# Performance work log

Measured on AMD Instinct MI355X. Metric: run time of the kernel, lower is better.

Reference implementation:

```python
import jax, jax.numpy as jnp
import numpy as np


def setup_inputs() -> dict:
    key = jax.random.key(0)
    k1, k2, k3 = jax.random.split(key, 3)
    B, N, M = 64, 1024, 1024
    src = jax.random.normal(k1, (B, 3, N), dtype=jnp.float32)
    tgt = jax.random.normal(k2, (B, 3, M), dtype=jnp.float32)
    scores = jax.random.normal(k3, (B, N, M), dtype=jnp.float32)
    return {"src": src, "tgt": tgt, "scores": scores}


def reference(src, tgt, scores):
    # softmax over the tgt-point axis (dim=2 in torch)
    p = jax.nn.softmax(scores, axis=2)                       # [B,N,M]
    # src_corr = tgt @ scores^T  -> soft correspondences in tgt for each src point
    src_corr = jnp.einsum('bdm,bnm->bdn', tgt, p)            # [B,3,N]
    src_mean = src.mean(axis=2, keepdims=True)               # [B,3,1]
    corr_mean = src_corr.mean(axis=2, keepdims=True)         # [B,3,1]
    src_c = src - src_mean
    corr_c = src_corr - corr_mean
    # cross-covariance H = src_centered @ src_corr_centered^T  -> [B,3,3]
    H = jnp.einsum('bdn,ben->bde', src_c, corr_c)
    U, S, Vh = jnp.linalg.svd(H)                             # batched 3x3 SVD
    V = jnp.swapaxes(Vh, -1, -2)
    Ut = jnp.swapaxes(U, -1, -2)
    R0 = V @ Ut                                              # candidate rotation
    det = jnp.linalg.det(R0)                                 # [B]
    # reflection fix: flip last column of V where det < 0 (reflect = diag(1,1,-1))
    flip = jnp.where(det < 0, -1.0, 1.0)                     # [B]
    ones = jnp.ones_like(flip)
    col_scale = jnp.stack([ones, ones, flip], axis=-1)[:, None, :]  # [B,1,3]
    R = (V * col_scale) @ Ut                                 # [B,3,3]
    t = (-R @ src_mean) + corr_mean                          # [B,3,1]
    return R, t.reshape(src.shape[0], 3)
```

## Files before the change

### kernel.cpp

```cpp
#include <hip/hip_runtime.h>
#include <math.h>

#define BATCH 64
#define NPTS  1024
#define MPTS  1024
#define ROWS_PER_BLOCK 8
#define BLOCKS_PER_BATCH (NPTS / ROWS_PER_BLOCK)

__global__ __launch_bounds__(512) void softmax_stats_kernel(
    const float* __restrict__ src,
    const float* __restrict__ tgt,
    const float* __restrict__ scores,
    float* __restrict__ partials)
{
    __shared__ float tgt_lds[3 * MPTS];
    __shared__ float part[ROWS_PER_BLOCK][16];

    const int tid  = threadIdx.x;
    const int lane = tid & 63;
    const int wave = tid >> 6;
    const int row0 = blockIdx.x * ROWS_PER_BLOCK;
    const int b    = row0 >> 10;

    {
        const float4* tgt4 = (const float4*)(tgt + (size_t)b * 3 * MPTS);
        float4* lds4 = (float4*)tgt_lds;
        for (int idx = tid; idx < 768; idx += 512)
            lds4[idx] = tgt4[idx];
    }
    __syncthreads();

    const int r = row0 + wave;
    const int n = r & (NPTS - 1);
    const float4* srow = (const float4*)(scores + (size_t)r * MPTS);

    float sum = 0.f, w0 = 0.f, w1 = 0.f, w2 = 0.f;
    float4 v[4];
    #pragma unroll
    for (int k = 0; k < 4; ++k) v[k] = srow[k * 64 + lane];
    #pragma unroll
    for (int k = 0; k < 4; ++k) {
        const int m4 = k * 64 + lane;
        float e0 = __expf(v[k].x);
        float e1 = __expf(v[k].y);
        float e2 = __expf(v[k].z);
        float e3 = __expf(v[k].w);
        sum += e0 + e1 + e2 + e3;
        float4 t0 = ((const float4*)(tgt_lds + 0 * MPTS))[m4];
        float4 t1 = ((const float4*)(tgt_lds + 1 * MPTS))[m4];
        float4 t2 = ((const float4*)(tgt_lds + 2 * MPTS))[m4];
        w0 += e0 * t0.x + e1 * t0.y + e2 * t0.z + e3 * t0.w;
        w1 += e0 * t1.x + e1 * t1.y + e2 * t1.z + e3 * t1.w;
        w2 += e0 * t2.x + e1 * t2.y + e2 * t2.z + e3 * t2.w;
    }
    #pragma unroll
    for (int off = 32; off >= 1; off >>= 1) {
        sum += __shfl_xor(sum, off);
        w0  += __shfl_xor(w0, off);
        w1  += __shfl_xor(w1, off);
        w2  += __shfl_xor(w2, off);
    }

    if (lane == 0) {
        const float inv = 1.0f / sum;
        const float c0 = w0 * inv, c1 = w1 * inv, c2 = w2 * inv;
        const float s0 = src[((size_t)b * 3 + 0) * NPTS + n];
        const float s1 = src[((size_t)b * 3 + 1) * NPTS + n];
        const float s2 = src[((size_t)b * 3 + 2) * NPTS + n];
        float* p = part[wave];
        p[0]  = s0; p[1]  = s1; p[2]  = s2;
        p[3]  = c0; p[4]  = c1; p[5]  = c2;
        p[6]  = s0 * c0; p[7]  = s0 * c1; p[8]  = s0 * c2;
        p[9]  = s1 * c0; p[10] = s1 * c1; p[11] = s1 * c2;
        p[12] = s2 * c0; p[13] = s2 * c1; p[14] = s2 * c2;
        p[15] = 0.f;
    }
    __syncthreads();

    if (tid < 16) {
        float a = 0.f;
        #pragma unroll
        for (int w = 0; w < ROWS_PER_BLOCK; ++w) a += part[w][tid];
        partials[(size_t)blockIdx.x * 16 + tid] = a;
    }
}

__global__ __launch_bounds__(64) void procrustes_kernel(
    const float* __restrict__ partials,
    float* __restrict__ out)
{
    const int b    = blockIdx.x;
    const int lane = threadIdx.x;

    float a[16];
    const float4* w4 = (const float4*)partials;
    #pragma unroll
    for (int q = 0; q < 4; ++q) {
        float4 x = w4[((size_t)b * 128 + lane) * 4 + q];
        float4 y = w4[((size_t)b * 128 + 64 + lane) * 4 + q];
        a[q * 4 + 0] = x.x + y.x;
        a[q * 4 + 1] = x.y + y.y;
        a[q * 4 + 2] = x.z + y.z;
        a[q * 4 + 3] = x.w + y.w;
    }
    #pragma unroll
    for (int off = 32; off >= 1; off >>= 1) {
        #pragma unroll
        for (int i = 0; i < 15; ++i) a[i] += __shfl_xor(a[i], off);
    }

    if (lane == 0) {
        const float invN = 1.0f / (float)NPTS;
        float mus[3], muc[3];
        #pragma unroll
        for (int d = 0; d < 3; ++d) { mus[d] = a[d] * invN; muc[d] = a[3 + d] * invN; }

        float Hm[3][3];
        #pragma unroll
        for (int d = 0; d < 3; ++d)
            #pragma unroll
            for (int e = 0; e < 3; ++e)
                Hm[d][e] = a[6 + d * 3 + e] - (float)NPTS * mus[d] * muc[e];

        float Bm[3][3], Vm[3][3];
        #pragma unroll
        for (int i = 0; i < 3; ++i)
            #pragma unroll
            for (int j = 0; j < 3; ++j) {
                Bm[i][j] = Hm[i][j];
                Vm[i][j] = (i == j) ? 1.f : 0.f;
            }

        const int PP[3] = {0, 0, 1};
        const int QQ[3] = {1, 2, 2};
        for (int sweep = 0; sweep < 8; ++sweep) {
            for (int rr = 0; rr < 3; ++rr) {
                const int p = PP[rr], q = QQ[rr];
                float aa = 0.f, bb = 0.f, c = 0.f;
                #pragma unroll
                for (int i = 0; i < 3; ++i) {
                    aa += Bm[i][p] * Bm[i][p];
                    bb += Bm[i][q] * Bm[i][q];
                    c  += Bm[i][p] * Bm[i][q];
                }
                if (fabsf(c) <= 1e-12f * sqrtf(aa * bb) || c == 0.f) continue;
                float tau = (bb - aa) / (2.f * c);
                float tt  = copysignf(1.f, tau) / (fabsf(tau) + sqrtf(1.f + tau * tau));
                float cs  = 1.f / sqrtf(1.f + tt * tt);
                float sn  = cs * tt;
                #pragma unroll
                for (int i = 0; i < 3; ++i) {
                    float bp = Bm[i][p], bq = Bm[i][q];
                    Bm[i][p] = cs * bp - sn * bq;
                    Bm[i][q] = sn * bp + cs * bq;
                    float vp = Vm[i][p], vq = Vm[i][q];
                    Vm[i][p] = cs * vp - sn * vq;
                    Vm[i][q] = sn * vp + cs * vq;
                }
            }
        }

        float sig[3];
        #pragma unroll
        for (int j = 0; j < 3; ++j)
            sig[j] = sqrtf(Bm[0][j] * Bm[0][j] + Bm[1][j] * Bm[1][j] + Bm[2][j] * Bm[2][j]);

        const int SP[3] = {0, 1, 0};
        const int SQ[3] = {1, 2, 1};
        for (int rr = 0; rr < 3; ++rr) {
            int p = SP[rr], q = SQ[rr];
            if (sig[p] < sig[q]) {
                float tsw = sig[p]; sig[p] = sig[q]; sig[q] = tsw;
                #pragma unroll
                for (int i = 0; i < 3; ++i) {
                    float t1 = Bm[i][p]; Bm[i][p] = Bm[i][q]; Bm[i][q] = t1;
                    float t2 = Vm[i][p]; Vm[i][p] = Vm[i][q]; Vm[i][q] = t2;
                }
            }
        }

        float Um[3][3];
        #pragma unroll
        for (int j = 0; j < 2; ++j) {
            float inv = 1.f / fmaxf(sig[j], 1e-30f);
            #pragma unroll
            for (int i = 0; i < 3; ++i) Um[i][j] = Bm[i][j] * inv;
        }
        if (sig[2] > 1e-6f * fmaxf(sig[0], 1e-30f)) {
            float inv = 1.f / sig[2];
            #pragma unroll
            for (int i = 0; i < 3; ++i) Um[i][2] = Bm[i][2] * inv;
        } else {
            float cx = Um[1][0] * Um[2][1] - Um[2][0] * Um[1][1];
            float cy = Um[2][0] * Um[0][1] - Um[0][0] * Um[2][1];
            float cz = Um[0][0] * Um[1][1] - Um[1][0] * Um[0][1];
            float inv = 1.f / fmaxf(sqrtf(cx * cx + cy * cy + cz * cz), 1e-30f);
            Um[0][2] = cx * inv; Um[1][2] = cy * inv; Um[2][2] = cz * inv;
        }

        float detU = Um[0][0] * (Um[1][1] * Um[2][2] - Um[1][2] * Um[2][1])
                   - Um[0][1] * (Um[1][0] * Um[2][2] - Um[1][2] * Um[2][0])
                   + Um[0][2] * (Um[1][0] * Um[2][1] - Um[1][1] * Um[2][0]);
        float detV = Vm[0][0] * (Vm[1][1] * Vm[2][2] - Vm[1][2] * Vm[2][1])
                   - Vm[0][1] * (Vm[1][0] * Vm[2][2] - Vm[1][2] * Vm[2][0])
                   + Vm[0][2] * (Vm[1][0] * Vm[2][1] - Vm[1][1] * Vm[2][0]);
        float flip = (detU * detV < 0.f) ? -1.f : 1.f;
        float fl[3] = {1.f, 1.f, flip};

        float R[3][3];
        #pragma unroll
        for (int i = 0; i < 3; ++i)
            #pragma unroll
            for (int j = 0; j < 3; ++j)
                R[i][j] = Vm[i][0] * fl[0] * Um[j][0]
                        + Vm[i][1] * fl[1] * Um[j][1]
                        + Vm[i][2] * fl[2] * Um[j][2];

        float* Rout = out + (size_t)b * 9;
        #pragma unroll
        for (int i = 0; i < 3; ++i)
            #pragma unroll
            for (int j = 0; j < 3; ++j)
                Rout[i * 3 + j] = R[i][j];

        float* tout = out + (size_t)BATCH * 9 + (size_t)b * 3;
        #pragma unroll
        for (int i = 0; i < 3; ++i)
            tout[i] = muc[i] - (R[i][0] * mus[0] + R[i][1] * mus[1] + R[i][2] * mus[2]);
    }
}

extern "C" void kernel_launch(void* const* d_in, const int* in_sizes, int n_in,
                              void* d_out, int out_size, void* d_ws, size_t ws_size,
                              hipStream_t stream) {
    const float* src    = (const float*)d_in[0];
    const float* tgt    = (const float*)d_in[1];
    const float* scores = (const float*)d_in[2];
    float* out      = (float*)d_out;
    float* partials = (float*)d_ws;

    const int nblocks = (BATCH * NPTS) / ROWS_PER_BLOCK;

    softmax_stats_kernel<<<dim3(nblocks), dim3(512), 0, stream>>>(
        src, tgt, scores, partials);

    procrustes_kernel<<<dim3(BATCH), dim3(64), 0, stream>>>(partials, out);
}
```

Before: 56.92 us.

## Make softmax waves persistent over 16 rows with double-buffered nontemporal loads

Each wave now handles 16 score rows instead of one, so each block covers 128 rows and only 512 blocks are launched instead of 8192. The tgt staging into LDS is amortized across many more rows, and src values for the block are staged in LDS too. Row loads are double-buffered with nontemporal hints, and statistics accumulate in registers per wave. The procrustes reduction is simplified to one value per lane followed by shuffles. The trade-off is lower parallelism: 512 blocks of 512 threads may not fill the GPU or hide memory latency as well as before.

```diff
diff --git a/kernel.cpp b/kernel.cpp
--- a/kernel.cpp
+++ b/kernel.cpp
@@ -4,83 +4,119 @@
 #define BATCH 64
 #define NPTS  1024
 #define MPTS  1024
-#define ROWS_PER_BLOCK 8
-#define BLOCKS_PER_BATCH (NPTS / ROWS_PER_BLOCK)
-
-__global__ __launch_bounds__(512) void softmax_stats_kernel(
+#define BLOCKS_PER_BATCH 8
+#define WAVES_PER_BLOCK  8
+#define ROWS_PER_WAVE    16
+
+typedef float f32x4 __attribute__((ext_vector_type(4)));
+
+__global__ __launch_bounds__(512, 4) void softmax_stats_kernel(
     const float* __restrict__ src,
     const float* __restrict__ tgt,
     const float* __restrict__ scores,
     float* __restrict__ partials)
 {
     __shared__ float tgt_lds[3 * MPTS];
-    __shared__ float part[ROWS_PER_BLOCK][16];
+    __shared__ float src_lds[3][BLOCKS_PER_BATCH * 16];
+    __shared__ float part[WAVES_PER_BLOCK][16];
 
     const int tid  = threadIdx.x;
     const int lane = tid & 63;
     const int wave = tid >> 6;
-    const int row0 = blockIdx.x * ROWS_PER_BLOCK;
-    const int b    = row0 >> 10;
+    const int b    = blockIdx.x >> 3;
+    const int bb   = blockIdx.x & 7;
+    const int nrows_blk = NPTS / BLOCKS_PER_BATCH;
+    const int n_base    = bb * nrows_blk;
+    const int n_wave    = n_base + wave * ROWS_PER_WAVE;
+
+    const f32x4* tgt_g = (const f32x4*)(tgt + (size_t)b * 3 * MPTS);
+    f32x4* tgt_l = (f32x4*)tgt_lds;
+
+    const float* srow0 = scores + ((size_t)b * NPTS + n_wave) * MPTS;
+    f32x4 va[4], vb[4];
+    #pragma unroll
+    for (int k = 0; k < 4; ++k)
+        va[k] = __builtin_nontemporal_load((const f32x4*)srow0 + k * 64 + lane);
 
     {
-        const float4* tgt4 = (const float4*)(tgt + (size_t)b * 3 * MPTS);
-        float4* lds4 = (float4*)tgt_lds;
-        for (int idx = tid; idx < 768; idx += 512)
-            lds4[idx] = tgt4[idx];
+        int i0 = tid, i1 = tid + 512;
+        tgt_l[i0] = tgt_g[i0];
+        if (i1 < 768) tgt_l[i1] = tgt_g[i1];
+        if (tid < 384) {
+            int d = tid >> 7, nn = tid & 127;
+            src_lds[d][nn] = src[((size_t)b * 3 + d) * NPTS + n_base + nn];
+        }
     }
     __syncthreads();
 
-    const int r = row0 + wave;
-    const int n = r & (NPTS - 1);
-    const float4* srow = (const float4*)(scores + (size_t)r * MPTS);
-
-    float sum = 0.f, w0 = 0.f, w1 = 0.f, w2 = 0.f;
-    float4 v[4];
+    float st[15];
     #pragma unroll
-    for (int k = 0; k < 4; ++k) v[k] = srow[k * 64 + lane];
-    #pragma unroll
-    for (int k = 0; k < 4; ++k) {
-        const int m4 = k * 64 + lane;
-        float e0 = __expf(v[k].x);
-        float e1 = __expf(v[k].y);
-        float e2 = __expf(v[k].z);
-        float e3 = __expf(v[k].w);
-        sum += e0 + e1 + e2 + e3;
-        float4 t0 = ((const float4*)(tgt_lds + 0 * MPTS))[m4];
-        float4 t1 = ((const float4*)(tgt_lds + 1 * MPTS))[m4];
-        float4 t2 = ((const float4*)(tgt_lds + 2 * MPTS))[m4];
-        w0 += e0 * t0.x + e1 * t0.y + e2 * t0.z + e3 * t0.w;
-        w1 += e0 * t1.x + e1 * t1.y + e2 * t1.z + e3 * t1.w;
-        w2 += e0 * t2.x + e1 * t2.y + e2 * t2.z + e3 * t2.w;
-    }
-    #pragma unroll
-    for (int off = 32; off >= 1; off >>= 1) {
-        sum += __shfl_xor(sum, off);
-        w0  += __shfl_xor(w0, off);
-        w1  += __shfl_xor(w1, off);
-        w2  += __shfl_xor(w2, off);
-    }
-
-    if (lane == 0) {
+    for (int i = 0; i < 15; ++i) st[i] = 0.f;
+
+    const f32x4* t0p = (const f32x4*)(tgt_lds + 0 * MPTS);
+    const f32x4* t1p = (const f32x4*)(tgt_lds + 1 * MPTS);
+    const f32x4* t2p = (const f32x4*)(tgt_lds + 2 * MPTS);
+
+    auto process = [&](const f32x4 v[4], int rr) {
+        float sum = 0.f, w0 = 0.f, w1 = 0.f, w2 = 0.f;
+        #pragma unroll
+        for (int k = 0; k < 4; ++k) {
+            const int m4 = k * 64 + lane;
+            float e0 = __expf(v[k].x);
+            float e1 = __expf(v[k].y);
+            float e2 = __expf(v[k].z);
+            float e3 = __expf(v[k].w);
+            sum += e0 + e1 + e2 + e3;
+            f32x4 t0 = t0p[m4], t1 = t1p[m4], t2 = t2p[m4];
+            w0 += e0 * t0.x + e1 * t0.y + e2 * t0.z + e3 * t0.w;
+            w1 += e0 * t1.x + e1 * t1.y + e2 * t1.z + e3 * t1.w;
+            w2 += e0 * t2.x + e1 * t2.y + e2 * t2.z + e3 * t2.w;
+        }
+        #pragma unroll
+        for (int off = 32; off >= 1; off >>= 1) {
+            sum += __shfl_xor(sum, off);
+            w0  += __shfl_xor(w0, off);
+            w1  += __shfl_xor(w1, off);
+            w2  += __shfl_xor(w2, off);
+        }
         const float inv = 1.0f / sum;
         const float c0 = w0 * inv, c1 = w1 * inv, c2 = w2 * inv;
-        const float s0 = src[((size_t)b * 3 + 0) * NPTS + n];
-        const float s1 = src[((size_t)b * 3 + 1) * NPTS + n];
-        const float s2 = src[((size_t)b * 3 + 2) * NPTS + n];
-        float* p = part[wave];
-        p[0]  = s0; p[1]  = s1; p[2]  = s2;
-        p[3]  = c0; p[4]  = c1; p[5]  = c2;
-        p[6]  = s0 * c0; p[7]  = s0 * c1; p[8]  = s0 * c2;
-        p[9]  = s1 * c0; p[10] = s1 * c1; p[11] = s1 * c2;
-        p[12] = s2 * c0; p[13] = s2 * c1; p[14] = s2 * c2;
-        p[15] = 0.f;
+        const int ln = wave * ROWS_PER_WAVE + rr;
+        const float s0 = src_lds[0][ln], s1 = src_lds[1][ln], s2 = src_lds[2][ln];
+        st[0] += s0; st[1] += s1; st[2] += s2;
+        st[3] += c0; st[4] += c1; st[5] += c2;
+        st[6]  += s0 * c0; st[7]  += s0 * c1; st[8]  += s0 * c2;
+        st[9]  += s1 * c0; st[10] += s1 * c1; st[11] += s1 * c2;
+        st[12] += s2 * c0; st[13] += s2 * c1; st[14] += s2 * c2;
+    };
+
+    const float* srow_base = scores + ((size_t)b * NPTS + n_wave) * MPTS;
+    for (int r = 0; r < ROWS_PER_WAVE; r += 2) {
+        const f32x4* rp1 = (const f32x4*)(srow_base + (size_t)(r + 1) * MPTS);
+        #pragma unroll
+        for (int k = 0; k < 4; ++k)
+            vb[k] = __builtin_nontemporal_load(rp1 + k * 64 + lane);
+        process(va, r);
+        if (r + 2 < ROWS_PER_WAVE) {
+            const f32x4* rp2 = (const f32x4*)(srow_base + (size_t)(r + 2) * MPTS);
+            #pragma unroll
+            for (int k = 0; k < 4; ++k)
+                va[k] = __builtin_nontemporal_load(rp2 + k * 64 + lane);
+        }
+        process(vb, r + 1);
+    }
+
+    if (lane == 0) {
+        #pragma unroll
+        for (int i = 0; i < 15; ++i) part[wave][i] = st[i];
+        part[wave][15] = 0.f;
     }
     __syncthreads();
 
     if (tid < 16) {
         float a = 0.f;
         #pragma unroll
-        for (int w = 0; w < ROWS_PER_BLOCK; ++w) a += part[w][tid];
+        for (int w = 0; w < WAVES_PER_BLOCK; ++w) a += part[w][tid];
         partials[(size_t)blockIdx.x * 16 + tid] = a;
     }
 }
@@ -92,22 +128,13 @@
     const int b    = blockIdx.x;
     const int lane = threadIdx.x;
 
-    float a[16];
-    const float4* w4 = (const float4*)partials;
+    float red = partials[(size_t)b * 128 + lane]
+              + partials[(size_t)b * 128 + 64 + lane];
+    red += __shfl_xor(red, 16);
+    red += __shfl_xor(red, 32);
+    float a[15];
     #pragma unroll
-    for (int q = 0; q < 4; ++q) {
-        float4 x = w4[((size_t)b * 128 + lane) * 4 + q];
-        float4 y = w4[((size_t)b * 128 + 64 + lane) * 4 + q];
-        a[q * 4 + 0] = x.x + y.x;
-        a[q * 4 + 1] = x.y + y.y;
-        a[q * 4 + 2] = x.z + y.z;
-        a[q * 4 + 3] = x.w + y.w;
-    }
-    #pragma unroll
-    for (int off = 32; off >= 1; off >>= 1) {
-        #pragma unroll
-        for (int i = 0; i < 15; ++i) a[i] += __shfl_xor(a[i], off);
-    }
+    for (int i = 0; i < 15; ++i) a[i] = __shfl(red, i);
 
     if (lane == 0) {
         const float invN = 1.0f / (float)NPTS;
@@ -239,9 +266,7 @@
     float* out      = (float*)d_out;
     float* partials = (float*)d_ws;
 
-    const int nblocks = (BATCH * NPTS) / ROWS_PER_BLOCK;
-
-    softmax_stats_kernel<<<dim3(nblocks), dim3(512), 0, stream>>>(
+    softmax_stats_kernel<<<dim3(BATCH * BLOCKS_PER_BATCH), dim3(512), 0, stream>>>(
         src, tgt, scores, partials);
 
     procrustes_kernel<<<dim3(BATCH), dim3(64), 0, stream>>>(partials, out);
```

Result: slower. 66.00 us (+16.0%).
